# Kernel tuning notes

Hardware: AMD Instinct MI355X
Metric: run time of the kernel (lower is better)

## Reference

```python
import jax, jax.numpy as jnp
import numpy as np
from jax import lax

N, CIN, COUT, T, V, S = 64, 64, 64, 256, 25, 3
REL = CIN // 8  # 8, per __init__ branch for in_channels=64


def setup_inputs() -> dict:
    key = jax.random.key(0)
    ks = jax.random.split(key, 22)
    rn = lambda i, shape, s=0.05: jax.random.normal(ks[i], shape, jnp.float32) * s
    return dict(
        x=jax.random.normal(ks[0], (N, CIN, T, V), jnp.float32),
        A=rn(1, (S, V, V), 0.2),                 # adaptive PA parameter
        alpha=jnp.asarray(0.1, jnp.float32),     # unit_gcn alpha (scalar)
        w1=rn(2, (S, REL, CIN)), b1=rn(3, (S, REL)),
        w2=rn(4, (S, REL, CIN)), b2=rn(5, (S, REL)),
        w3=rn(6, (S, COUT, CIN)), b3=rn(7, (S, COUT)),
        w4=rn(8, (S, COUT, REL)), b4=rn(9, (S, COUT)),
        pm_w1=rn(10, (S, REL, 2 * REL)), pm_b1=rn(11, (S, REL)),
        pm_w2=rn(12, (S, REL, REL)), pm_b2=rn(13, (S, REL)),
        dw_w=rn(14, (S, REL, 1, 3, 3)),          # depthwise 3x3, groups=REL
        proj_w=rn(15, (S, COUT, REL)),           # aux_proj, no bias
        beta=rn(16, (S,), 0.01), gamma=rn(17, (S,), 0.01),
        bn_w=jnp.ones((COUT,), jnp.float32), bn_b=jnp.zeros((COUT,), jnp.float32),
    )


def _sorgc(x, Ai, alpha, w1, b1, w2, b2, w3, b3, w4, b4,
           pw1, pb1, pw2, pb2, dww, pjw, beta, gamma):
    # x: (N, C, T, V)
    xm = x.mean(axis=2)                                            # (N,C,V) -- 1x1 conv is linear, so conv then mean == mean then conv
    x1 = jnp.einsum('ncv,rc->nrv', xm, w1) + b1[:, None]           # (N,R,V)
    x2 = jnp.einsum('ncv,rc->nrv', xm, w2) + b2[:, None]
    x3 = jnp.einsum('nctv,oc->notv', x, w3) + b3[:, None, None]    # (N,O,T,V)
    q1 = jnp.tanh(x1[:, :, :, None] - x2[:, :, None, :])           # (N,R,V,V)
    psi = jnp.broadcast_to(x2[:, :, :, None], q1.shape)
    phi = jnp.broadcast_to(x2[:, :, None, :], q1.shape)
    pair = jnp.concatenate([psi, phi], axis=1)                     # (N,2R,V,V)
    h = jax.nn.relu(jnp.einsum('npuv,rp->nruv', pair, pw1) + pb1[:, None, None])
    q2 = jnp.einsum('npuv,rp->nruv', h, pw2) + pb2[:, None, None]
    q_all = q1 + gamma * q2
    R = (jnp.einsum('nruv,or->nouv', q_all, w4) + b4[:, None, None]) * alpha + Ai[None, None]
    # aux branch: depthwise 3x3 conv -> avgpool3x3 (count_include_pad) -> tanh -> 1x1 proj
    Ra = lax.conv_general_dilated(q1, dww, (1, 1), [(1, 1), (1, 1)],
                                  dimension_numbers=('NCHW', 'OIHW', 'NCHW'),
                                  feature_group_count=q1.shape[1])
    Ra = lax.reduce_window(Ra, 0.0, lax.add, (1, 1, 3, 3), (1, 1, 1, 1),
                           [(0, 0), (0, 0), (1, 1), (1, 1)]) / 9.0
    Ra = jnp.tanh(Ra)
    Ra = jnp.einsum('nruv,or->nouv', Ra, pjw)                      # (N,O,V,V)
    R = R + beta * Ra
    return jnp.einsum('ncuv,nctv->nctu', R, x3)                    # (N,O,T,V)


def reference(x, A, alpha, w1, b1, w2, b2, w3, b3, w4, b4,
              pm_w1, pm_b1, pm_w2, pm_b2, dw_w, proj_w, beta, gamma, bn_w, bn_b):
    y = None
    for i in range(S):
        z = _sorgc(x, A[i], alpha, w1[i], b1[i], w2[i], b2[i], w3[i], b3[i],
                   w4[i], b4[i], pm_w1[i], pm_b1[i], pm_w2[i], pm_b2[i],
                   dw_w[i], proj_w[i], beta[i], gamma[i])
        y = z if y is None else y + z
    # BatchNorm2d (training-mode batch statistics), eps=1e-5
    mu = y.mean(axis=(0, 2, 3), keepdims=True)
    var = y.var(axis=(0, 2, 3), keepdims=True)
    y = (y - mu) * lax.rsqrt(var + 1e-5) * bn_w[None, :, None, None] + bn_b[None, :, None, None]
    y = y + x  # residual (in_channels == out_channels -> identity down)
    return jax.nn.relu(y)
```

## Files before the change

### kernel.cpp

```cpp
#include <hip/hip_runtime.h>


#define WS_R_BYTE   409600

typedef __attribute__((ext_vector_type(8))) short bf16x8;
typedef __attribute__((ext_vector_type(4))) float f32x4;
typedef __attribute__((ext_vector_type(2))) float f32x2;

static __device__ __forceinline__ unsigned short f2bf(float f) {
    unsigned int u = __float_as_uint(f);
    u += 0x7fff + ((u >> 16) & 1);
    return (unsigned short)(u >> 16);
}
static __device__ __forceinline__ float bf2f(unsigned short s) {
    return __uint_as_float(((unsigned int)s) << 16);
}

__global__ __launch_bounds__(256) void k_xm(const float* __restrict__ x,
                                            float* __restrict__ ws) {
    int idx = blockIdx.x * 256 + threadIdx.x;
    int n = idx / 1600;
    int cv = idx % 1600;
    int c = cv / 25, v = cv % 25;
    const float* xp = x + (n * 64 + c) * 6400 + v;
    float s = 0.f;
    #pragma unroll 8
    for (int t = 0; t < 256; t++) s += xp[t * 25];
    ws[idx] = s * (1.f / 256.f);
}

__global__ __launch_bounds__(512) void k_small(
    const float* __restrict__ ws, unsigned short* __restrict__ Rg,
    const float* __restrict__ A, const float* __restrict__ alphap,
    const float* __restrict__ w1, const float* __restrict__ b1,
    const float* __restrict__ w2, const float* __restrict__ b2,
    const float* __restrict__ w4, const float* __restrict__ b4,
    const float* __restrict__ pw1, const float* __restrict__ pb1,
    const float* __restrict__ pw2, const float* __restrict__ pb2,
    const float* __restrict__ dww, const float* __restrict__ pjw,
    const float* __restrict__ beta, const float* __restrict__ gamma) {
    __shared__ float sm[15000];
    const int tid = threadIdx.x;
    const int s = blockIdx.x >> 6;
    const int n = blockIdx.x & 63;
    const float alpha = alphap[0];
    const float gam = gamma[s], bet = beta[s];

    for (int i = tid; i < 1600; i += 512) sm[5000 + i] = ws[n * 1600 + i];
    __syncthreads();

    for (int i = tid; i < 400; i += 512) {
        int half = i / 200, j = i % 200;
        int r = j / 25, k = j % 25;
        const float* w = (half ? w2 : w1) + (s * 8 + r) * 64;
        float acc = (half ? b2 : b1)[s * 8 + r];
        for (int c = 0; c < 64; c++) acc += w[c] * sm[5000 + c * 25 + k];
        sm[6600 + i] = acc;
    }
    __syncthreads();

    for (int i = tid; i < 5400; i += 512) {
        if (i < 5000) {
            int r = i / 625, uv = i % 625, u = uv / 25, v = uv % 25;
            sm[i] = tanhf(sm[6600 + r * 25 + u] - sm[6800 + r * 25 + v]);
        } else {
            int i2 = i - 5000;
            int half = i2 / 200, j = i2 % 200;
            int r = j / 25, k = j % 25;
            float acc = 0.f;
            for (int p = 0; p < 8; p++)
                acc += pw1[(s * 8 + r) * 16 + half * 8 + p] * sm[6800 + p * 25 + k];
            sm[7000 + i2] = acc;
        }
    }
    __syncthreads();

    for (int i = tid; i < 5000; i += 512) {
        int r = i / 625, uv = i % 625, u = uv / 25, v = uv % 25;
        float t = sm[7000 + r * 25 + u] + sm[7200 + r * 25 + v] + pb1[s * 8 + r];
        sm[10000 + i] = t > 0.f ? t : 0.f;
    }
    __syncthreads();

    for (int i = tid; i < 5000; i += 512) {
        int r = i / 625, uv = i % 625;
        float q2 = pb2[s * 8 + r];
        for (int p = 0; p < 8; p++)
            q2 += pw2[(s * 8 + r) * 8 + p] * sm[10000 + p * 625 + uv];
        sm[5000 + i] = sm[i] + gam * q2;
    }
    __syncthreads();

    for (int i = tid; i < 5000; i += 512) {
        int r = i / 625, uv = i % 625, u = uv / 25, v = uv % 25;
        float acc = 0.f;
        for (int di = 0; di < 3; di++) {
            int uu = u + di - 1;
            if (uu < 0 || uu > 24) continue;
            for (int dj = 0; dj < 3; dj++) {
                int vv = v + dj - 1;
                if (vv < 0 || vv > 24) continue;
                acc += sm[r * 625 + uu * 25 + vv] * dww[(s * 8 + r) * 9 + di * 3 + dj];
            }
        }
        sm[10000 + i] = acc;
    }
    __syncthreads();

    for (int i = tid; i < 5000; i += 512) {
        int r = i / 625, uv = i % 625, u = uv / 25, v = uv % 25;
        float acc = 0.f;
        for (int di = 0; di < 3; di++) {
            int uu = u + di - 1;
            if (uu < 0 || uu > 24) continue;
            for (int dj = 0; dj < 3; dj++) {
                int vv = v + dj - 1;
                if (vv < 0 || vv > 24) continue;
                acc += sm[10000 + r * 625 + uu * 25 + vv];
            }
        }
        sm[i] = tanhf(acc * (1.f / 9.f));
    }
    __syncthreads();

    unsigned short* Rb = Rg + (unsigned)((s * 64 + n) * 64) * 704;
    for (int i = tid; i < 40000; i += 512) {
        int o = i / 625, vu = i % 625, vv = vu / 25, uu = vu % 25;
        int quv = uu * 25 + vv;
        float mn = b4[s * 64 + o], aux = 0.f;
        for (int r = 0; r < 8; r++) {
            mn  += w4[(s * 64 + o) * 8 + r] * sm[5000 + r * 625 + quv];
            aux += pjw[(s * 64 + o) * 8 + r] * sm[r * 625 + quv];
        }
        Rb[o * 704 + vv * 28 + uu] = f2bf(mn * alpha + A[s * 625 + quv] + bet * aux);
    }
    for (int i = tid; i < 64 * 25 * 3; i += 512) {
        int o = i / 75, rem = i % 75, vv = rem / 3, uu = 25 + rem % 3;
        Rb[o * 704 + vv * 28 + uu] = 0;
    }
}

__global__ __launch_bounds__(256, 3) void k_main(
    const float* __restrict__ x, const float* __restrict__ w3,
    const float* __restrict__ b3, const unsigned short* __restrict__ Rg,
    float* __restrict__ out, float* __restrict__ bnacc) {
    __shared__ __align__(16) unsigned short xb[400 * 64];
    const int tid  = threadIdx.x;
    const int n    = blockIdx.x >> 4;
    const int t0   = (blockIdx.x & 15) * 16;
    const int lane = tid & 63;
    const int w    = tid >> 6;
    const int ln15 = lane & 15;
    const int q    = lane >> 4;
    const int og   = w * 16 + ln15;

    {
        const float* xbase = x + n * 409600 + t0 * 25;
        #pragma unroll 5
        for (int k = 0; k < 25; k++) {
            int i  = tid + k * 256;
            int tv = i % 400;
            int cq = i / 400;
            const float* p = xbase + cq * 4 * 6400 + tv;
            ushort4 h;
            h.x = f2bf(p[0]); h.y = f2bf(p[6400]); h.z = f2bf(p[12800]); h.w = f2bf(p[19200]);
            int addr = tv * 64 + (((cq >> 1) ^ (tv & 7)) << 3) + ((cq & 1) << 2);
            *(ushort4*)&xb[addr] = h;
        }
    }
    __syncthreads();

    f32x2 yacc[25][2];
    #pragma unroll
    for (int u = 0; u < 25; u++) {
        yacc[u][0] = (f32x2){0.f, 0.f};
        yacc[u][1] = (f32x2){0.f, 0.f};
    }

    for (int s = 0; s < 3; s++) {
        bf16x8 bfr[2];
        {
            const float* wp = w3 + (s * 64 + og) * 64;
            #pragma unroll
            for (int ks = 0; ks < 2; ks++)
                #pragma unroll
                for (int j = 0; j < 8; j++)
                    bfr[ks][j] = (short)f2bf(wp[ks * 32 + q * 8 + j]);
        }
        const float bias = b3[s * 64 + og];
        const unsigned short* rrbase =
            Rg + ((unsigned)((s * 64 + n) * 64 + og)) * 704;

        for (int v = 0; v < 25; v++) {
            const int row = ln15 * 25 + v;
            const int sw  = row & 7;
            bf16x8 a0 = *(const bf16x8*)&xb[row * 64 + ((q ^ sw) << 3)];
            bf16x8 a1 = *(const bf16x8*)&xb[row * 64 + (((4 + q) ^ sw) << 3)];
            f32x4 cc; cc[0] = bias; cc[1] = bias; cc[2] = bias; cc[3] = bias;
            cc = __builtin_amdgcn_mfma_f32_16x16x32_bf16(a0, bfr[0], cc, 0, 0, 0);
            cc = __builtin_amdgcn_mfma_f32_16x16x32_bf16(a1, bfr[1], cc, 0, 0, 0);
            f32x2 c0; c0[0] = cc[0]; c0[1] = cc[1];
            f32x2 c1; c1[0] = cc[2]; c1[1] = cc[3];

            const unsigned short* rr = rrbase + v * 28;
            #pragma unroll
            for (int ug = 0; ug < 6; ug++) {
                ushort4 r4 = *(const ushort4*)(rr + ug * 4);
                float f0 = bf2f(r4.x), f1 = bf2f(r4.y);
                float f2 = bf2f(r4.z), f3 = bf2f(r4.w);
                yacc[ug * 4 + 0][0] += f0 * c0; yacc[ug * 4 + 0][1] += f0 * c1;
                yacc[ug * 4 + 1][0] += f1 * c0; yacc[ug * 4 + 1][1] += f1 * c1;
                yacc[ug * 4 + 2][0] += f2 * c0; yacc[ug * 4 + 2][1] += f2 * c1;
                yacc[ug * 4 + 3][0] += f3 * c0; yacc[ug * 4 + 3][1] += f3 * c1;
            }
            float f24 = bf2f(rr[24]);
            yacc[24][0] += f24 * c0;
            yacc[24][1] += f24 * c1;
        }
    }

    float* op = out + (n * 64 + og) * 6400 + t0 * 25;
    #pragma unroll
    for (int h = 0; h < 2; h++) {
        #pragma unroll
        for (int c = 0; c < 2; c++) {
            float* opr = op + (q * 4 + h * 2 + c) * 25;
            #pragma unroll
            for (int ug = 0; ug < 6; ug++) {
                float st[4] = {yacc[ug * 4 + 0][h][c], yacc[ug * 4 + 1][h][c],
                               yacc[ug * 4 + 2][h][c], yacc[ug * 4 + 3][h][c]};
                __builtin_memcpy(opr + ug * 4, st, 16);
            }
            opr[24] = yacc[24][h][c];
        }
    }

    float s1 = 0.f, s2 = 0.f;
    #pragma unroll
    for (int u = 0; u < 25; u++) {
        #pragma unroll
        for (int h = 0; h < 2; h++) {
            f32x2 yv = yacc[u][h];
            s1 += yv[0] + yv[1];
            s2 += yv[0] * yv[0] + yv[1] * yv[1];
        }
    }
    s1 += __shfl_xor(s1, 16); s1 += __shfl_xor(s1, 32);
    s2 += __shfl_xor(s2, 16); s2 += __shfl_xor(s2, 32);
    if (q == 0) {
        atomicAdd(&bnacc[og * 16], s1);
        atomicAdd(&bnacc[1024 + og * 16], s2);
    }
}

__global__ __launch_bounds__(256) void k_final(
    float* __restrict__ out, const float* __restrict__ x,
    const float* __restrict__ bnacc,
    const float* __restrict__ bnw, const float* __restrict__ bnb) {
    const int idx4 = blockIdx.x * 256 + threadIdx.x;
    const int o = (idx4 / 1600) & 63;
    const float cnt = 1.f / 409600.f;
    float mean = bnacc[o * 16] * cnt;
    float var = bnacc[1024 + o * 16] * cnt - mean * mean;
    float inv = rsqrtf(var + 1e-5f);
    float sc = bnw[o] * inv;
    float sh = bnb[o] - mean * sc;
    float4 y = ((const float4*)out)[idx4];
    float4 xv = ((const float4*)x)[idx4];
    y.x = fmaxf(y.x * sc + sh + xv.x, 0.f);
    y.y = fmaxf(y.y * sc + sh + xv.y, 0.f);
    y.z = fmaxf(y.z * sc + sh + xv.z, 0.f);
    y.w = fmaxf(y.w * sc + sh + xv.w, 0.f);
    ((float4*)out)[idx4] = y;
}

extern "C" void kernel_launch(void* const* d_in, const int* in_sizes, int n_in,
                              void* d_out, int out_size, void* d_ws, size_t ws_size,
                              hipStream_t stream) {
    const float* x     = (const float*)d_in[0];
    const float* A     = (const float*)d_in[1];
    const float* alpha = (const float*)d_in[2];
    const float* w1    = (const float*)d_in[3];
    const float* b1    = (const float*)d_in[4];
    const float* w2    = (const float*)d_in[5];
    const float* b2    = (const float*)d_in[6];
    const float* w3    = (const float*)d_in[7];
    const float* b3    = (const float*)d_in[8];
    const float* w4    = (const float*)d_in[9];
    const float* b4    = (const float*)d_in[10];
    const float* pw1   = (const float*)d_in[11];
    const float* pb1   = (const float*)d_in[12];
    const float* pw2   = (const float*)d_in[13];
    const float* pb2   = (const float*)d_in[14];
    const float* dww   = (const float*)d_in[15];
    const float* pjw   = (const float*)d_in[16];
    const float* beta  = (const float*)d_in[17];
    const float* gamma = (const float*)d_in[18];
    const float* bnw   = (const float*)d_in[19];
    const float* bnb   = (const float*)d_in[20];
    float* out = (float*)d_out;
    float* ws  = (float*)d_ws;
    unsigned short* wsR = (unsigned short*)((char*)d_ws + WS_R_BYTE);
    float* wsBN = ws;

    k_xm<<<400, 256, 0, stream>>>(x, ws);
    k_small<<<192, 512, 0, stream>>>(ws, wsR, A, alpha, w1, b1, w2, b2,
                                     w4, b4, pw1, pb1, pw2, pb2, dww, pjw,
                                     beta, gamma);
    hipMemsetAsync(wsBN, 0, 8192, stream);
    k_main<<<1024, 256, 0, stream>>>(x, w3, b3, wsR, out, wsBN);
    k_final<<<25600, 256, 0, stream>>>(out, x, wsBN, bnw, bnb);
}
```

Measured before the change: 523.4 us.

## Move graph aggregation einsum onto MFMA via bf16 x3 staged in LDS

The per-vertex aggregation y[o,t,u] = sum_v R[o,u,v]·x3[o,t,v] is moved from scalar FMA loops onto bf16 MFMA instructions. x3 is computed with MFMA, packed to bf16 pairs, and staged through a reused 64KB LDS buffer; R is read from a new row-major padded layout (28 stride, zero-filled). This trades FMA throughput pressure for extra LDS traffic, per-stage re-staging of x, more barriers, extra bf16 rounding of x3, and occupancy lowered to 2 blocks per SM. The BN statistics reduction now uses a full-wave shuffle per output channel.

```diff
diff --git a/kernel.cpp b/kernel.cpp
--- a/kernel.cpp
+++ b/kernel.cpp
@@ -5,16 +5,19 @@
 
 typedef __attribute__((ext_vector_type(8))) short bf16x8;
 typedef __attribute__((ext_vector_type(4))) float f32x4;
-typedef __attribute__((ext_vector_type(2))) float f32x2;
+typedef __attribute__((ext_vector_type(2))) unsigned int u32x2;
+typedef __attribute__((ext_vector_type(4))) unsigned int u32x4;
 
 static __device__ __forceinline__ unsigned short f2bf(float f) {
     unsigned int u = __float_as_uint(f);
     u += 0x7fff + ((u >> 16) & 1);
     return (unsigned short)(u >> 16);
 }
-static __device__ __forceinline__ float bf2f(unsigned short s) {
-    return __uint_as_float(((unsigned int)s) << 16);
-}
+static __device__ __forceinline__ unsigned pk2(float lo, float hi) {
+    return (unsigned)f2bf(lo) | ((unsigned)f2bf(hi) << 16);
+}
+
+union BFRU { bf16x8 v; unsigned u[4]; u32x2 d[2]; };
 
 __global__ __launch_bounds__(256) void k_xm(const float* __restrict__ x,
                                             float* __restrict__ ws) {
@@ -123,61 +126,66 @@
     }
     __syncthreads();
 
-    unsigned short* Rb = Rg + (unsigned)((s * 64 + n) * 64) * 704;
-    for (int i = tid; i < 40000; i += 512) {
-        int o = i / 625, vu = i % 625, vv = vu / 25, uu = vu % 25;
-        int quv = uu * 25 + vv;
-        float mn = b4[s * 64 + o], aux = 0.f;
-        for (int r = 0; r < 8; r++) {
-            mn  += w4[(s * 64 + o) * 8 + r] * sm[5000 + r * 625 + quv];
-            aux += pjw[(s * 64 + o) * 8 + r] * sm[r * 625 + quv];
-        }
-        Rb[o * 704 + vv * 28 + uu] = f2bf(mn * alpha + A[s * 625 + quv] + bet * aux);
-    }
-    for (int i = tid; i < 64 * 25 * 3; i += 512) {
-        int o = i / 75, rem = i % 75, vv = rem / 3, uu = 25 + rem % 3;
-        Rb[o * 704 + vv * 28 + uu] = 0;
-    }
-}
-
-__global__ __launch_bounds__(256, 3) void k_main(
+    unsigned short* Rb = Rg + (unsigned)((s * 64 + n)) * 44800u;
+    for (int i = tid; i < 44800; i += 512) {
+        int o = i / 700, uv = i % 700, uu = uv / 28, vv = uv % 28;
+        unsigned short val = 0;
+        if (vv < 25) {
+            int quv = uu * 25 + vv;
+            float mn = b4[s * 64 + o], aux = 0.f;
+            for (int r = 0; r < 8; r++) {
+                mn  += w4[(s * 64 + o) * 8 + r] * sm[5000 + r * 625 + quv];
+                aux += pjw[(s * 64 + o) * 8 + r] * sm[r * 625 + quv];
+            }
+            val = f2bf(mn * alpha + A[s * 625 + quv] + bet * aux);
+        }
+        Rb[i] = val;
+    }
+}
+
+__global__ __launch_bounds__(256, 2) void k_main(
     const float* __restrict__ x, const float* __restrict__ w3,
     const float* __restrict__ b3, const unsigned short* __restrict__ Rg,
     float* __restrict__ out, float* __restrict__ bnacc) {
-    __shared__ __align__(16) unsigned short xb[400 * 64];
+    __shared__ __align__(16) unsigned char smem[65536];
+    unsigned short* xb  = (unsigned short*)smem;
+    unsigned*       x3w = (unsigned*)smem;
+    unsigned short* x3s = (unsigned short*)smem;
+
     const int tid  = threadIdx.x;
     const int n    = blockIdx.x >> 4;
     const int t0   = (blockIdx.x & 15) * 16;
     const int lane = tid & 63;
     const int w    = tid >> 6;
-    const int ln15 = lane & 15;
+    const int a    = lane & 15;
     const int q    = lane >> 4;
-    const int og   = w * 16 + ln15;
-
-    {
-        const float* xbase = x + n * 409600 + t0 * 25;
-        #pragma unroll 5
-        for (int k = 0; k < 25; k++) {
-            int i  = tid + k * 256;
-            int tv = i % 400;
-            int cq = i / 400;
-            const float* p = xbase + cq * 4 * 6400 + tv;
-            ushort4 h;
-            h.x = f2bf(p[0]); h.y = f2bf(p[6400]); h.z = f2bf(p[12800]); h.w = f2bf(p[19200]);
-            int addr = tv * 64 + (((cq >> 1) ^ (tv & 7)) << 3) + ((cq & 1) << 2);
-            *(ushort4*)&xb[addr] = h;
-        }
-    }
-    __syncthreads();
-
-    f32x2 yacc[25][2];
+    const int og   = w * 16 + a;
+
+    f32x4 yacc[16][2];
     #pragma unroll
-    for (int u = 0; u < 25; u++) {
-        yacc[u][0] = (f32x2){0.f, 0.f};
-        yacc[u][1] = (f32x2){0.f, 0.f};
+    for (int k = 0; k < 16; k++) {
+        yacc[k][0] = (f32x4){0.f, 0.f, 0.f, 0.f};
+        yacc[k][1] = (f32x4){0.f, 0.f, 0.f, 0.f};
     }
 
     for (int s = 0; s < 3; s++) {
+        {
+            const float* xbase = x + n * 409600 + t0 * 25;
+            #pragma unroll 5
+            for (int k = 0; k < 25; k++) {
+                int i  = tid + k * 256;
+                int tv = i % 400;
+                int cq = i / 400;
+                const float* p = xbase + cq * 4 * 6400 + tv;
+                ushort4 h;
+                h.x = f2bf(p[0]); h.y = f2bf(p[6400]);
+                h.z = f2bf(p[12800]); h.w = f2bf(p[19200]);
+                int addr = tv * 64 + (((cq >> 1) ^ (tv & 7)) << 3) + ((cq & 1) << 2);
+                *(ushort4*)&xb[addr] = h;
+            }
+        }
+        __syncthreads();
+
         bf16x8 bfr[2];
         {
             const float* wp = w3 + (s * 64 + og) * 64;
@@ -188,68 +196,111 @@
                     bfr[ks][j] = (short)f2bf(wp[ks * 32 + q * 8 + j]);
         }
         const float bias = b3[s * 64 + og];
-        const unsigned short* rrbase =
-            Rg + ((unsigned)((s * 64 + n) * 64 + og)) * 704;
-
-        for (int v = 0; v < 25; v++) {
-            const int row = ln15 * 25 + v;
+
+        unsigned x3pk[13][4];
+        #pragma unroll
+        for (int i = 0; i < 12; i++) {
+            f32x4 ca, cb;
+            {
+                const int row = a * 25 + 2 * i;
+                const int sw  = row & 7;
+                bf16x8 a0 = *(const bf16x8*)&xb[row * 64 + ((q ^ sw) << 3)];
+                bf16x8 a1 = *(const bf16x8*)&xb[row * 64 + (((4 + q) ^ sw) << 3)];
+                f32x4 c0; c0[0] = bias; c0[1] = bias; c0[2] = bias; c0[3] = bias;
+                c0 = __builtin_amdgcn_mfma_f32_16x16x32_bf16(a0, bfr[0], c0, 0, 0, 0);
+                ca = __builtin_amdgcn_mfma_f32_16x16x32_bf16(a1, bfr[1], c0, 0, 0, 0);
+            }
+            {
+                const int row = a * 25 + 2 * i + 1;
+                const int sw  = row & 7;
+                bf16x8 a0 = *(const bf16x8*)&xb[row * 64 + ((q ^ sw) << 3)];
+                bf16x8 a1 = *(const bf16x8*)&xb[row * 64 + (((4 + q) ^ sw) << 3)];
+                f32x4 c0; c0[0] = bias; c0[1] = bias; c0[2] = bias; c0[3] = bias;
+                c0 = __builtin_amdgcn_mfma_f32_16x16x32_bf16(a0, bfr[0], c0, 0, 0, 0);
+                cb = __builtin_amdgcn_mfma_f32_16x16x32_bf16(a1, bfr[1], c0, 0, 0, 0);
+            }
+            #pragma unroll
+            for (int r = 0; r < 4; r++) x3pk[i][r] = pk2(ca[r], cb[r]);
+        }
+        {
+            const int row = a * 25 + 24;
             const int sw  = row & 7;
             bf16x8 a0 = *(const bf16x8*)&xb[row * 64 + ((q ^ sw) << 3)];
             bf16x8 a1 = *(const bf16x8*)&xb[row * 64 + (((4 + q) ^ sw) << 3)];
-            f32x4 cc; cc[0] = bias; cc[1] = bias; cc[2] = bias; cc[3] = bias;
-            cc = __builtin_amdgcn_mfma_f32_16x16x32_bf16(a0, bfr[0], cc, 0, 0, 0);
-            cc = __builtin_amdgcn_mfma_f32_16x16x32_bf16(a1, bfr[1], cc, 0, 0, 0);
-            f32x2 c0; c0[0] = cc[0]; c0[1] = cc[1];
-            f32x2 c1; c1[0] = cc[2]; c1[1] = cc[3];
-
-            const unsigned short* rr = rrbase + v * 28;
+            f32x4 c0; c0[0] = bias; c0[1] = bias; c0[2] = bias; c0[3] = bias;
+            c0 = __builtin_amdgcn_mfma_f32_16x16x32_bf16(a0, bfr[0], c0, 0, 0, 0);
+            c0 = __builtin_amdgcn_mfma_f32_16x16x32_bf16(a1, bfr[1], c0, 0, 0, 0);
             #pragma unroll
-            for (int ug = 0; ug < 6; ug++) {
-                ushort4 r4 = *(const ushort4*)(rr + ug * 4);
-                float f0 = bf2f(r4.x), f1 = bf2f(r4.y);
-                float f2 = bf2f(r4.z), f3 = bf2f(r4.w);
-                yacc[ug * 4 + 0][0] += f0 * c0; yacc[ug * 4 + 0][1] += f0 * c1;
-                yacc[ug * 4 + 1][0] += f1 * c0; yacc[ug * 4 + 1][1] += f1 * c1;
-                yacc[ug * 4 + 2][0] += f2 * c0; yacc[ug * 4 + 2][1] += f2 * c1;
-                yacc[ug * 4 + 3][0] += f3 * c0; yacc[ug * 4 + 3][1] += f3 * c1;
-            }
-            float f24 = bf2f(rr[24]);
-            yacc[24][0] += f24 * c0;
-            yacc[24][1] += f24 * c1;
-        }
-    }
-
-    float* op = out + (n * 64 + og) * 6400 + t0 * 25;
+            for (int r = 0; r < 4; r++) x3pk[12][r] = pk2(c0[r], 0.f);
+        }
+        __syncthreads();
+
+        #pragma unroll
+        for (int r = 0; r < 4; r++) {
+            unsigned* dst = &x3w[og * 256 + (q * 4 + r) * 16];
+            u32x4 w0, w1, w2, wd;
+            w0[0] = x3pk[0][r];  w0[1] = x3pk[1][r];
+            w0[2] = x3pk[2][r];  w0[3] = x3pk[3][r];
+            w1[0] = x3pk[4][r];  w1[1] = x3pk[5][r];
+            w1[2] = x3pk[6][r];  w1[3] = x3pk[7][r];
+            w2[0] = x3pk[8][r];  w2[1] = x3pk[9][r];
+            w2[2] = x3pk[10][r]; w2[3] = x3pk[11][r];
+            wd[0] = x3pk[12][r]; wd[1] = 0u; wd[2] = 0u; wd[3] = 0u;
+            *(u32x4*)(dst)      = w0;
+            *(u32x4*)(dst + 4)  = w1;
+            *(u32x4*)(dst + 8)  = w2;
+            *(u32x4*)(dst + 12) = wd;
+        }
+        __syncthreads();
+
+        const unsigned short* Rsn = Rg + (unsigned)((s * 64 + n)) * 44800u;
+        #pragma unroll
+        for (int k = 0; k < 16; k++) {
+            const int o = w * 16 + k;
+            const unsigned short* Ro = Rsn + o * 700;
+            bf16x8 B = *(const bf16x8*)&x3s[o * 512 + a * 32 + q * 8];
+            BFRU A0, A1;
+            A0.d[0] = *(const u32x2*)(Ro + a * 28 + q * 8);
+            A0.d[1] = *(const u32x2*)(Ro + a * 28 + q * 8 + 4);
+            const int u1 = (a < 9) ? (16 + a) : 0;
+            A1.d[0] = *(const u32x2*)(Ro + u1 * 28 + q * 8);
+            A1.d[1] = *(const u32x2*)(Ro + u1 * 28 + q * 8 + 4);
+            yacc[k][0] = __builtin_amdgcn_mfma_f32_16x16x32_bf16(A0.v, B, yacc[k][0], 0, 0, 0);
+            yacc[k][1] = __builtin_amdgcn_mfma_f32_16x16x32_bf16(A1.v, B, yacc[k][1], 0, 0, 0);
+        }
+        __syncthreads();
+    }
+
+    float* outb = out + (unsigned)(n * 64) * 6400u + (t0 + a) * 25;
     #pragma unroll
-    for (int h = 0; h < 2; h++) {
-        #pragma unroll
-        for (int c = 0; c < 2; c++) {
-            float* opr = op + (q * 4 + h * 2 + c) * 25;
-            #pragma unroll
-            for (int ug = 0; ug < 6; ug++) {
-                float st[4] = {yacc[ug * 4 + 0][h][c], yacc[ug * 4 + 1][h][c],
-                               yacc[ug * 4 + 2][h][c], yacc[ug * 4 + 3][h][c]};
-                __builtin_memcpy(opr + ug * 4, st, 16);
-            }
-            opr[24] = yacc[24][h][c];
-        }
-    }
-
-    float s1 = 0.f, s2 = 0.f;
-    #pragma unroll
-    for (int u = 0; u < 25; u++) {
-        #pragma unroll
-        for (int h = 0; h < 2; h++) {
-            f32x2 yv = yacc[u][h];
-            s1 += yv[0] + yv[1];
-            s2 += yv[0] * yv[0] + yv[1] * yv[1];
-        }
-    }
-    s1 += __shfl_xor(s1, 16); s1 += __shfl_xor(s1, 32);
-    s2 += __shfl_xor(s2, 16); s2 += __shfl_xor(s2, 32);
-    if (q == 0) {
-        atomicAdd(&bnacc[og * 16], s1);
-        atomicAdd(&bnacc[1024 + og * 16], s2);
+    for (int k = 0; k < 16; k++) {
+        const int o = w * 16 + k;
+        float* op = outb + o * 6400;
+        float s1 = 0.f, s2 = 0.f;
+        #pragma unroll
+        for (int r = 0; r < 4; r++) {
+            float vv = yacc[k][0][r];
+            op[q * 4 + r] = vv;
+            s1 += vv; s2 += vv * vv;
+        }
+        #pragma unroll
+        for (int r = 0; r < 4; r++) {
+            int u = 16 + q * 4 + r;
+            if (u < 25) {
+                float vv = yacc[k][1][r];
+                op[u] = vv;
+                s1 += vv; s2 += vv * vv;
+            }
+        }
+        #pragma unroll
+        for (int off = 1; off < 64; off <<= 1) {
+            s1 += __shfl_xor(s1, off);
+            s2 += __shfl_xor(s2, off);
+        }
+        if (lane == 0) {
+            atomicAdd(&bnacc[o * 16], s1);
+            atomicAdd(&bnacc[1024 + o * 16], s2);
+        }
     }
 }
 
```

Measured after the change: 563.8 us. 7.7% more time.
